# Kernel tuning notes

Measured on AMD Instinct MI355X. Metric: run time of the kernel, lower is better.

## Reference

```python
import jax, jax.numpy as jnp
import numpy as np

IMG_X, IMG_Y = 1333.0, 402.0   # image_size
MIN_SIZE = 16.0
NMS_THRESH = 0.7
PRE = 12000                    # n_train_pre_nms
POST = 2000                    # n_train_post_nms
HH, WW, A = 83, 25, 9          # 1333//16, 402//16, anchors per cell
N_ANCH = HH * WW * A           # 18675
B = 16


def setup_inputs() -> dict:
    key = jax.random.key(0)
    k1, k2, k3, k4, k5, k6 = jax.random.split(key, 6)
    # realistic anchor boxes inside the image
    xc = jax.random.uniform(k1, (N_ANCH,)) * IMG_X
    yc = jax.random.uniform(k2, (N_ANCH,)) * IMG_Y
    bw = jax.random.uniform(k3, (N_ANCH,)) * 240.0 + 16.0
    bh = jax.random.uniform(k4, (N_ANCH,)) * 120.0 + 16.0
    anchor_boxes = jnp.stack([xc - 0.5 * bw, yc - 0.5 * bh, xc + 0.5 * bw, yc + 0.5 * bh], axis=1)
    rpn_cls_score = jax.random.normal(k5, (B, N_ANCH * 2), dtype=jnp.float32)
    rpn_bbox_pred = jax.random.normal(k6, (B, N_ANCH, 4), dtype=jnp.float32) * 0.2
    return dict(anchor_boxes=anchor_boxes, rpn_cls_score=rpn_cls_score,
                rpn_bbox_pred=rpn_bbox_pred, rpn_cls_loss=jnp.zeros((1,), jnp.float32),
                rpn_bbox_loss=jnp.zeros((1,), jnp.float32))


def _decode(anchor_boxes, rpn_bbox_pred):
    ah = anchor_boxes[:, 3] - anchor_boxes[:, 1]
    aw = anchor_boxes[:, 2] - anchor_boxes[:, 0]
    acy = anchor_boxes[:, 1] + 0.5 * ah
    acx = anchor_boxes[:, 0] + 0.5 * aw
    dx = rpn_bbox_pred[..., 0]
    dy = rpn_bbox_pred[..., 1]
    dw = rpn_bbox_pred[..., 2]
    dh = rpn_bbox_pred[..., 3]
    cy = dy * ah + acy
    cx = dx * aw + acx
    h = jnp.exp(dh) * ah
    w = jnp.exp(dw) * aw
    # clip: x coords to [0, image_size[0]], y coords to [0, image_size[1]] (as in source)
    x1 = jnp.clip(cx - 0.5 * w, 0.0, IMG_X)
    y1 = jnp.clip(cy - 0.5 * h, 0.0, IMG_Y)
    x2 = jnp.clip(cx + 0.5 * w, 0.0, IMG_X)
    y2 = jnp.clip(cy + 0.5 * h, 0.0, IMG_Y)
    return jnp.stack([x1, y1, x2, y2], axis=-1)  # [N,4] broadcast over batch -> [B,N,4]


def _nms_one(roi, score):
    # roi: [N,4], score: [N]
    hs = roi[:, 3] - roi[:, 1]
    ws = roi[:, 2] - roi[:, 0]
    valid = (hs >= MIN_SIZE) & (ws >= MIN_SIZE)
    s = jnp.where(valid, score, -jnp.inf)
    idx = jnp.argsort(-s)[:PRE]          # score-descending, top pre_nms; invalid sink to end
    boxes = roi[idx]                      # score-sorted candidate boxes [PRE,4]
    vp = valid[idx]                       # which slots are real (passed size filter)
    # source quirk: order = order.argsort()[::-1] -> NMS visits boxes by DESCENDING
    # original-anchor-index; invalid slots get key -1 so they come last.
    seq_key = jnp.where(vp, idx, -1)
    perm = jnp.argsort(-seq_key)          # positions into score-sorted arrays, visit order
    x1, y1, x2, y2 = boxes[:, 0], boxes[:, 1], boxes[:, 2], boxes[:, 3]
    areas = (x2 - x1 + 1.0) * (y2 - y1 + 1.0)

    def step(alive, _):
        a_seq = alive[perm]
        any_alive = a_seq.any()
        j = perm[jnp.argmax(a_seq)]       # first surviving box in visit order
        xx1 = jnp.maximum(x1[j], x1)
        yy1 = jnp.maximum(y1[j], y1)
        xx2 = jnp.minimum(x2[j], x2)
        yy2 = jnp.minimum(y2[j], y2)
        inter = jnp.maximum(0.0, xx2 - xx1 + 1.0) * jnp.maximum(0.0, yy2 - yy1 + 1.0)
        ovr = inter / (areas[j] + areas - inter)
        alive = alive & jnp.where(any_alive, ovr <= NMS_THRESH, True)  # j kills itself (ovr=1)
        return alive, jnp.where(any_alive, j, -1)

    _, keep = jax.lax.scan(step, vp, None, length=POST)   # up to post_nms kept positions
    kmask = keep >= 0
    out = jnp.where(kmask[:, None], boxes[jnp.maximum(keep, 0)], 0.0)  # padded [POST,4]
    return out, kmask


def reference(anchor_boxes, rpn_cls_score, rpn_bbox_pred, rpn_cls_loss, rpn_bbox_loss):
    bsz = rpn_cls_score.shape[0]
    # objectness = view(B, 83, 25, 9, 2)[..., 1]
    score = rpn_cls_score.reshape(bsz, HH, WW, A, 2)[..., 1].reshape(bsz, -1)
    roi = _decode(anchor_boxes, rpn_bbox_pred)            # [B,N,4]
    rois, mask = jax.vmap(_nms_one)(roi, score)           # [B,POST,4], [B,POST]
    return rois, mask
```

## Files before the change

kernel.cpp:

```cpp
#include <hip/hip_runtime.h>
#include <math.h>

#define N_ANCHN 18675
#define NPAD    18688
#define BATCH   16
#define PRE     12000
#define CPAD    12032
#define WPB     188
#define POST    2000
#define NMS_T   0.7f
#define IMGX    1333.0f
#define IMGY    402.0f
#define MINSZ   16.0f
#define NBUCK   256
#define KINV    0x007FFFFFu
#define MLCAP   12288

typedef unsigned long long u64;

__device__ __forceinline__ unsigned key_of(float f) {
  unsigned u = __float_as_uint(f);
  return (u & 0x80000000u) ? ~u : (u | 0x80000000u);
}

__device__ __forceinline__ float iou_ref(float ax1, float ay1, float ax2, float ay2, float aar,
                                         float bx1, float by1, float bx2, float by2, float bar) {
  float xx1 = fmaxf(ax1, bx1);
  float yy1 = fmaxf(ay1, by1);
  float xx2 = fminf(ax2, bx2);
  float yy2 = fminf(ay2, by2);
  float iw = fmaxf(0.0f, __fadd_rn(__fsub_rn(xx2, xx1), 1.0f));
  float ih = fmaxf(0.0f, __fadd_rn(__fsub_rn(yy2, yy1), 1.0f));
  float inter = __fmul_rn(iw, ih);
  return __fdiv_rn(inter, __fsub_rn(__fadd_rn(aar, bar), inter));
}

__device__ __forceinline__ bool hit_test(float ix1, float iy1, float ix2, float iy2, float iar,
                                         float jx1, float jy1, float jx2, float jy2, float jar) {
  float xx1 = fmaxf(ix1, jx1);
  float yy1 = fmaxf(iy1, jy1);
  float xx2 = fminf(ix2, jx2);
  float yy2 = fminf(iy2, jy2);
  float iw = fmaxf(0.0f, __fadd_rn(__fsub_rn(xx2, xx1), 1.0f));
  float ih = fmaxf(0.0f, __fadd_rn(__fsub_rn(yy2, yy1), 1.0f));
  float inter = __fmul_rn(iw, ih);
  float S = __fadd_rn(iar, jar);
  if (inter >= __fmul_rn(0.43f, S)) return true;
  if (inter <= __fmul_rn(0.395f, S)) return false;
  return __fdiv_rn(inter, __fsub_rn(S, inter)) > NMS_T;
}

__device__ __forceinline__ void emit_hit(int lo, int hi, u64* diagb, unsigned* rcb,
                                         unsigned short* rtb, int L) {
  if ((hi >> 6) == (lo >> 6)) {
    atomicOr(&diagb[(size_t)(lo >> 6) * 64 + (lo & 63)], 1ull << (hi & 63));
  } else {
    unsigned slot = atomicAdd(&rcb[lo], 1u);
    if ((int)slot < L) rtb[(size_t)lo * L + slot] = (unsigned short)hi;
  }
}

__device__ __forceinline__ void decode_one(
    const float* __restrict__ anchors, const float* __restrict__ cls,
    const float* __restrict__ bbox, int b, int i,
    float& x1, float& y1, float& x2, float& y2, unsigned& key) {
  float4 A = *(const float4*)(anchors + (size_t)i * 4);
  float ah = __fsub_rn(A.w, A.y);
  float aw = __fsub_rn(A.z, A.x);
  float acy = __fadd_rn(A.y, __fmul_rn(0.5f, ah));
  float acx = __fadd_rn(A.x, __fmul_rn(0.5f, aw));

  float4 P = *(const float4*)(bbox + ((size_t)b * N_ANCHN + i) * 4);
  float dx = P.x, dy = P.y, dw = P.z, dh = P.w;

  float cy = __fadd_rn(__fmul_rn(dy, ah), acy);
  float cx = __fadd_rn(__fmul_rn(dx, aw), acx);
  float eh = (float)exp((double)dh);
  float ew = (float)exp((double)dw);
  float h = __fmul_rn(eh, ah);
  float w = __fmul_rn(ew, aw);

  x1 = fminf(fmaxf(__fsub_rn(cx, __fmul_rn(0.5f, w)), 0.0f), IMGX);
  y1 = fminf(fmaxf(__fsub_rn(cy, __fmul_rn(0.5f, h)), 0.0f), IMGY);
  x2 = fminf(fmaxf(__fadd_rn(cx, __fmul_rn(0.5f, w)), 0.0f), IMGX);
  y2 = fminf(fmaxf(__fadd_rn(cy, __fmul_rn(0.5f, h)), 0.0f), IMGY);

  bool valid = (__fsub_rn(y2, y1) >= MINSZ) && (__fsub_rn(x2, x1) >= MINSZ);
  float s = valid ? cls[(size_t)b * (2 * N_ANCHN) + 2 * i + 1] : -INFINITY;
  key = key_of(s);
}

__global__ __launch_bounds__(256) void decode_kernel(
    const float* __restrict__ anchors, const float* __restrict__ cls,
    const float* __restrict__ bbox,
    float* __restrict__ bx1, float* __restrict__ by1,
    float* __restrict__ bx2, float* __restrict__ by2,
    unsigned* __restrict__ keys,
    u64* __restrict__ diag, unsigned* __restrict__ rowcnt) {
  const int bx = blockIdx.x;
  const int b = blockIdx.y;
  if (bx == gridDim.x - 1) {
    u64* dz = diag + (size_t)b * WPB * 64;
    for (int i = threadIdx.x; i < WPB * 64; i += 256) dz[i] = 0ull;
    unsigned* rz = rowcnt + (size_t)b * CPAD;
    for (int i = threadIdx.x; i < CPAD; i += 256) rz[i] = 0u;
    return;
  }
  int i = bx * 256 + threadIdx.x;
  if (i >= N_ANCHN) return;
  float x1, y1, x2, y2; unsigned k;
  decode_one(anchors, cls, bbox, b, i, x1, y1, x2, y2, k);
  size_t o = (size_t)b * NPAD + i;
  bx1[o] = x1; by1[o] = y1; bx2[o] = x2; by2[o] = y2;
  keys[o] = k;
}

__global__ __launch_bounds__(1024) void prepsort_kernel(
    const unsigned* __restrict__ keys,
    const float* __restrict__ bx1, const float* __restrict__ by1,
    const float* __restrict__ bx2, const float* __restrict__ by2,
    float* __restrict__ cx1, float* __restrict__ cy1,
    float* __restrict__ cx2, float* __restrict__ cy2,
    float* __restrict__ car, int* __restrict__ ncand,
    float* __restrict__ sx1, float* __restrict__ sy1,
    float* __restrict__ sx2, float* __restrict__ sy2,
    float* __restrict__ sar, int* __restrict__ sperm,
    float* __restrict__ wminx1, float* __restrict__ wmaxx2) {
  const int b = blockIdx.x;
  const int tid = threadIdx.x;
  const int lane = tid & 63;
  const int wv = tid >> 6;
  __shared__ unsigned hist[16][256];
  __shared__ unsigned mh[256];
  __shared__ unsigned wsum[16];
  __shared__ unsigned bh[NBUCK];
  __shared__ unsigned boff[NBUCK];
  __shared__ unsigned char fb[NPAD];
  __shared__ unsigned short mlist[MLCAP];
  __shared__ unsigned sh_prefix, sh_k, sh_n, sh_mcount;
  const unsigned* kb = keys + (size_t)b * NPAD;

  if (tid == 0) { sh_prefix = 0u; sh_k = PRE; sh_mcount = 0u; }
  __syncthreads();

  {
    for (int idx = tid; idx < 16 * 256; idx += 1024) ((unsigned*)hist)[idx] = 0u;
    __syncthreads();
    for (int i = tid; i < N_ANCHN; i += 1024)
      atomicAdd(&hist[wv][kb[i] >> 24], 1u);
    __syncthreads();
    if (tid < 256) {
      unsigned s = 0;
#pragma unroll
      for (int q = 0; q < 16; ++q) s += hist[q][tid];
      mh[tid] = s;
    }
    __syncthreads();
    if (tid == 0) {
      unsigned kk = sh_k, cum = 0;
      for (int d = 255; d >= 0; --d) {
        unsigned c = mh[d];
        if (cum + c >= kk) { sh_k = kk - cum; sh_prefix = (unsigned)d << 24; break; }
        cum += c;
      }
    }
    __syncthreads();
  }

  {
    unsigned b0 = sh_prefix >> 24;
    for (int i = tid; i < N_ANCHN; i += 1024) {
      if ((kb[i] >> 24) == b0) {
        unsigned p = atomicAdd(&sh_mcount, 1u);
        if (p < MLCAP) mlist[p] = (unsigned short)i;
      }
    }
  }
  __syncthreads();
  const bool useList = (sh_mcount <= (unsigned)MLCAP);
  const unsigned mcount = min(sh_mcount, (unsigned)MLCAP);

  for (int level = 1; level < 4; ++level) {
    const int shift = 24 - 8 * level;
    for (int idx = tid; idx < 16 * 256; idx += 1024) ((unsigned*)hist)[idx] = 0u;
    __syncthreads();
    unsigned pre = sh_prefix;
    if (useList) {
      for (int idx = tid; idx < (int)mcount; idx += 1024) {
        unsigned k = kb[mlist[idx]];
        if ((k >> (shift + 8)) == (pre >> (shift + 8)))
          atomicAdd(&hist[wv][(k >> shift) & 255u], 1u);
      }
    } else {
      for (int i = tid; i < N_ANCHN; i += 1024) {
        unsigned k = kb[i];
        if ((k >> (shift + 8)) == (pre >> (shift + 8)))
          atomicAdd(&hist[wv][(k >> shift) & 255u], 1u);
      }
    }
    __syncthreads();
    if (tid < 256) {
      unsigned s = 0;
#pragma unroll
      for (int q = 0; q < 16; ++q) s += hist[q][tid];
      mh[tid] = s;
    }
    __syncthreads();
    if (tid == 0) {
      unsigned kk = sh_k, cum = 0;
      for (int d = 255; d >= 0; --d) {
        unsigned c = mh[d];
        if (cum + c >= kk) { sh_k = kk - cum; sh_prefix = pre | ((unsigned)d << shift); break; }
        cum += c;
      }
    }
    __syncthreads();
  }
  const unsigned T = sh_prefix;
  const unsigned slots = sh_k;

  const int SEG = (N_ANCHN + 1023) / 1024;

  {
    int i0 = tid * SEG, i1 = min(N_ANCHN, i0 + SEG);
    unsigned cnt = 0;
    for (int i = i0; i < i1; ++i) cnt += (kb[i] == T) ? 1u : 0u;
    unsigned v = cnt;
#pragma unroll
    for (int d = 1; d < 64; d <<= 1) {
      unsigned y = __shfl_up(v, d, 64);
      if (lane >= d) v += y;
    }
    if (lane == 63) wsum[wv] = v;
    __syncthreads();
    if (tid == 0) {
      unsigned acc = 0;
#pragma unroll
      for (int q = 0; q < 16; ++q) { unsigned t = wsum[q]; wsum[q] = acc; acc += t; }
    }
    __syncthreads();
    unsigned r = wsum[wv] + v - cnt;
    for (int i = i0; i < i1; ++i) {
      unsigned k = kb[i];
      bool tie = (k == T);
      bool cand = (k > T) || (tie && T > KINV && r < slots);
      if (tie) r++;
      fb[i] = cand ? (unsigned char)1 : (unsigned char)0;
    }
  }
  __syncthreads();

  const float* X1 = bx1 + (size_t)b * NPAD;
  const float* Y1 = by1 + (size_t)b * NPAD;
  const float* X2 = bx2 + (size_t)b * NPAD;
  const float* Y2 = by2 + (size_t)b * NPAD;
  {
    int j0 = tid * SEG, j1 = min(N_ANCHN, j0 + SEG);
    unsigned cnt = 0;
    for (int j = j0; j < j1; ++j) cnt += fb[N_ANCHN - 1 - j];
    unsigned v = cnt;
#pragma unroll
    for (int d = 1; d < 64; d <<= 1) {
      unsigned y = __shfl_up(v, d, 64);
      if (lane >= d) v += y;
    }
    if (lane == 63) wsum[wv] = v;
    __syncthreads();
    if (tid == 0) {
      unsigned acc = 0;
#pragma unroll
      for (int q = 0; q < 16; ++q) { unsigned t = wsum[q]; wsum[q] = acc; acc += t; }
      sh_n = acc;
    }
    __syncthreads();
    unsigned p = wsum[wv] + v - cnt;
    if (tid == 0) ncand[b] = (int)sh_n;
    float* CX1 = cx1 + (size_t)b * CPAD;
    float* CY1 = cy1 + (size_t)b * CPAD;
    float* CX2 = cx2 + (size_t)b * CPAD;
    float* CY2 = cy2 + (size_t)b * CPAD;
    float* CAR = car + (size_t)b * CPAD;
    for (int j = j0; j < j1; ++j) {
      int i = N_ANCHN - 1 - j;
      if (fb[i]) {
        float x1v = X1[i], y1v = Y1[i], x2v = X2[i], y2v = Y2[i];
        CX1[p] = x1v; CY1[p] = y1v; CX2[p] = x2v; CY2[p] = y2v;
        CAR[p] = __fmul_rn(__fadd_rn(__fsub_rn(x2v, x1v), 1.0f),
                           __fadd_rn(__fsub_rn(y2v, y1v), 1.0f));
        p++;
      }
    }
  }
  __syncthreads();
  const int n = (int)sh_n;

  const float scale = (float)NBUCK / 1334.0f;
  const float* CX1 = cx1 + (size_t)b * CPAD;
  const float* CY1 = cy1 + (size_t)b * CPAD;
  const float* CX2 = cx2 + (size_t)b * CPAD;
  const float* CY2 = cy2 + (size_t)b * CPAD;
  const float* CAR = car + (size_t)b * CPAD;
  float* SX1 = sx1 + (size_t)b * CPAD;
  float* SY1 = sy1 + (size_t)b * CPAD;
  float* SX2 = sx2 + (size_t)b * CPAD;
  float* SY2 = sy2 + (size_t)b * CPAD;
  float* SAR = sar + (size_t)b * CPAD;
  int* SP = sperm + (size_t)b * CPAD;

  if (tid < NBUCK) bh[tid] = 0u;
  __syncthreads();
  for (int i = tid; i < n; i += 1024) {
    int q = (int)(CX1[i] * scale);
    q = q < 0 ? 0 : (q > NBUCK - 1 ? NBUCK - 1 : q);
    atomicAdd(&bh[q], 1u);
  }
  __syncthreads();
  if (tid < 64) {
    unsigned carry = 0;
    for (int c = 0; c < 4; ++c) {
      unsigned own = bh[c * 64 + tid];
      unsigned v = own;
      for (int d = 1; d < 64; d <<= 1) {
        unsigned y = __shfl_up(v, d, 64);
        if (tid >= d) v += y;
      }
      boff[c * 64 + tid] = carry + v - own;
      carry += __shfl(v, 63, 64);
    }
  }
  __syncthreads();
  for (int i = tid; i < n; i += 1024) {
    float x1v = CX1[i];
    int q = (int)(x1v * scale);
    q = q < 0 ? 0 : (q > NBUCK - 1 ? NBUCK - 1 : q);
    unsigned p = atomicAdd(&boff[q], 1u);
    SX1[p] = x1v; SY1[p] = CY1[i]; SX2[p] = CX2[i]; SY2[p] = CY2[i];
    SAR[p] = CAR[i]; SP[p] = i;
  }
  for (int i = n + tid; i < CPAD; i += 1024) {
    SX1[i] = 1e30f; SY1[i] = 1e30f; SX2[i] = -1e30f; SY2[i] = -1e30f;
    SAR[i] = 1.0f; SP[i] = 0;
  }
  __syncthreads();
  for (int w = wv; w < WPB; w += 16) {
    float mn = SX1[64 * w + lane];
    float mx = SX2[64 * w + lane];
#pragma unroll
    for (int d = 32; d > 0; d >>= 1) {
      mn = fminf(mn, __shfl_xor(mn, d, 64));
      mx = fmaxf(mx, __shfl_xor(mx, d, 64));
    }
    if (lane == 0) {
      wminx1[(size_t)b * WPB + w] = mn;
      wmaxx2[(size_t)b * WPB + w] = mx;
    }
  }
}

__global__ __launch_bounds__(256) void build_kernel(
    const float* __restrict__ sx1, const float* __restrict__ sy1,
    const float* __restrict__ sx2, const float* __restrict__ sy2,
    const float* __restrict__ sar, const int* __restrict__ sperm,
    const int* __restrict__ ncand,
    const float* __restrict__ wminx1, const float* __restrict__ wmaxx2,
    u64* __restrict__ diagT, unsigned* __restrict__ rowcnt,
    unsigned short* __restrict__ rows_t, int L) {
  const int R = blockIdx.x, G0 = blockIdx.y, b = blockIdx.z;
  const int n = ncand[b];
  if (64 * R >= n) return;
  if (16 * G0 + 15 < R) return;
  const float* WMN = wminx1 + (size_t)b * WPB;
  const float rlim = __fadd_rn(wmaxx2[(size_t)b * WPB + R], 2.0f);
  {
    const int wlo = max(16 * G0, R);
    if (WMN[wlo] > __fadd_rn(rlim, 5.25f)) return;
  }

  const float* SX1 = sx1 + (size_t)b * CPAD;
  const float* SY1 = sy1 + (size_t)b * CPAD;
  const float* SX2 = sx2 + (size_t)b * CPAD;
  const float* SY2 = sy2 + (size_t)b * CPAD;
  const float* SAR = sar + (size_t)b * CPAD;
  const int* SP = sperm + (size_t)b * CPAD;

  const int t = threadIdx.x, lane = t & 63, q = t >> 6;

  __shared__ float4 rbv[64];
  __shared__ float2 ras[64];
  if (t < 64) {
    int i = 64 * R + t;
    rbv[t] = make_float4(SX1[i], SY1[i], SX2[i], SY2[i]);
  } else if (t < 128) {
    int i = 64 * R + (t - 64);
    ras[t - 64] = make_float2(SAR[i], __int_as_float(SP[i]));
  }
  const float rx2own = SX2[64 * R + lane];
  __syncthreads();

  const int w0 = 16 * G0 + 4 * q;
  const float wmn0 = WMN[min(w0 + 0, WPB - 1)];
  const float wmn1 = WMN[min(w0 + 1, WPB - 1)];
  const float wmn2 = WMN[min(w0 + 2, WPB - 1)];
  const float wmn3 = WMN[min(w0 + 3, WPB - 1)];
  const bool v0 = (w0 + 0 < WPB) && (w0 + 0 >= R) && (wmn0 <= rlim);
  const bool v1 = (w0 + 1 < WPB) && (w0 + 1 >= R) && (wmn1 <= rlim);
  const bool v2 = (w0 + 2 < WPB) && (w0 + 2 >= R) && (wmn2 <= rlim);
  const bool v3 = (w0 + 3 < WPB) && (w0 + 3 >= R) && (wmn3 <= rlim);
  if (!(v0 | v1 | v2 | v3)) return;

  float c0x1 = 1e30f, c0y1 = 0.f, c0x2 = 0.f, c0y2 = 0.f, c0ar = 1.f; int c0sp = 0;
  float c1x1 = 1e30f, c1y1 = 0.f, c1x2 = 0.f, c1y2 = 0.f, c1ar = 1.f; int c1sp = 0;
  float c2x1 = 1e30f, c2y1 = 0.f, c2x2 = 0.f, c2y2 = 0.f, c2ar = 1.f; int c2sp = 0;
  float c3x1 = 1e30f, c3y1 = 0.f, c3x2 = 0.f, c3y2 = 0.f, c3ar = 1.f; int c3sp = 0;
  if (v0) { int j = 64 * (w0 + 0) + lane;
    c0x1 = SX1[j]; c0y1 = SY1[j]; c0x2 = SX2[j]; c0y2 = SY2[j]; c0ar = SAR[j]; c0sp = SP[j]; }
  if (v1) { int j = 64 * (w0 + 1) + lane;
    c1x1 = SX1[j]; c1y1 = SY1[j]; c1x2 = SX2[j]; c1y2 = SY2[j]; c1ar = SAR[j]; c1sp = SP[j]; }
  if (v2) { int j = 64 * (w0 + 2) + lane;
    c2x1 = SX1[j]; c2y1 = SY1[j]; c2x2 = SX2[j]; c2y2 = SY2[j]; c2ar = SAR[j]; c2sp = SP[j]; }
  if (v3) { int j = 64 * (w0 + 3) + lane;
    c3x1 = SX1[j]; c3y1 = SY1[j]; c3x2 = SX2[j]; c3y2 = SY2[j]; c3ar = SAR[j]; c3sp = SP[j]; }

  const float wmnlo = v0 ? wmn0 : (v1 ? wmn1 : (v2 ? wmn2 : wmn3));
  u64 a = __ballot(rx2own >= __fsub_rn(wmnlo, 2.0f));
  if (!a) return;

  const float wmn0m2 = __fsub_rn(wmn0, 2.0f);
  const float wmn1m2 = __fsub_rn(wmn1, 2.0f);
  const float wmn2m2 = __fsub_rn(wmn2, 2.0f);
  const float wmn3m2 = __fsub_rn(wmn3, 2.0f);

  u64* diagb = diagT + (size_t)b * WPB * 64;
  unsigned* rcb = rowcnt + (size_t)b * CPAD;
  unsigned short* rtb = rows_t + (size_t)b * L * CPAD;

  const bool diagIn = (w0 <= R) & (R <= w0 + 3);
  if (!diagIn) {
    int k = (int)__builtin_ctzll(a);
    float4 RB = rbv[k];
    float2 AS = ras[k];
    while (true) {
      a &= a - 1;
      const int kn = a ? (int)__builtin_ctzll(a) : 0;
      const float4 RBn = rbv[kn];
      const float2 ASn = ras[kn];
      const float rx2k = RB.z;
      const float rark = AS.x;
      const int rsp = __float_as_int(AS.y);
      if (v0 && rx2k >= wmn0m2 &&
          hit_test(RB.x, RB.y, RB.z, RB.w, rark, c0x1, c0y1, c0x2, c0y2, c0ar))
        emit_hit(min(rsp, c0sp), max(rsp, c0sp), diagb, rcb, rtb, L);
      if (v1 && rx2k >= wmn1m2 &&
          hit_test(RB.x, RB.y, RB.z, RB.w, rark, c1x1, c1y1, c1x2, c1y2, c1ar))
        emit_hit(min(rsp, c1sp), max(rsp, c1sp), diagb, rcb, rtb, L);
      if (v2 && rx2k >= wmn2m2 &&
          hit_test(RB.x, RB.y, RB.z, RB.w, rark, c2x1, c2y1, c2x2, c2y2, c2ar))
        emit_hit(min(rsp, c2sp), max(rsp, c2sp), diagb, rcb, rtb, L);
      if (v3 && rx2k >= wmn3m2 &&
          hit_test(RB.x, RB.y, RB.z, RB.w, rark, c3x1, c3y1, c3x2, c3y2, c3ar))
        emit_hit(min(rsp, c3sp), max(rsp, c3sp), diagb, rcb, rtb, L);
      if (!a) break;
      RB = RBn; AS = ASn;
    }
  } else {
    const bool g0 = (w0 + 0 > R), e0 = (w0 + 0 == R);
    const bool g1 = (w0 + 1 > R), e1 = (w0 + 1 == R);
    const bool g2 = (w0 + 2 > R), e2 = (w0 + 2 == R);
    const bool g3 = (w0 + 3 > R), e3 = (w0 + 3 == R);
    int k = (int)__builtin_ctzll(a);
    float4 RB = rbv[k];
    float2 AS = ras[k];
    while (true) {
      a &= a - 1;
      const int kn = a ? (int)__builtin_ctzll(a) : 0;
      const float4 RBn = rbv[kn];
      const float2 ASn = ras[kn];
      const float rx2k = RB.z;
      const float rark = AS.x;
      const int rsp = __float_as_int(AS.y);
      if (v0 && rx2k >= wmn0m2) {
        bool dd = g0 | (e0 & (lane > k));
        if (dd && hit_test(RB.x, RB.y, RB.z, RB.w, rark, c0x1, c0y1, c0x2, c0y2, c0ar))
          emit_hit(min(rsp, c0sp), max(rsp, c0sp), diagb, rcb, rtb, L);
      }
      if (v1 && rx2k >= wmn1m2) {
        bool dd = g1 | (e1 & (lane > k));
        if (dd && hit_test(RB.x, RB.y, RB.z, RB.w, rark, c1x1, c1y1, c1x2, c1y2, c1ar))
          emit_hit(min(rsp, c1sp), max(rsp, c1sp), diagb, rcb, rtb, L);
      }
      if (v2 && rx2k >= wmn2m2) {
        bool dd = g2 | (e2 & (lane > k));
        if (dd && hit_test(RB.x, RB.y, RB.z, RB.w, rark, c2x1, c2y1, c2x2, c2y2, c2ar))
          emit_hit(min(rsp, c2sp), max(rsp, c2sp), diagb, rcb, rtb, L);
      }
      if (v3 && rx2k >= wmn3m2) {
        bool dd = g3 | (e3 & (lane > k));
        if (dd && hit_test(RB.x, RB.y, RB.z, RB.w, rark, c3x1, c3y1, c3x2, c3y2, c3ar))
          emit_hit(min(rsp, c3sp), max(rsp, c3sp), diagb, rcb, rtb, L);
      }
      if (!a) break;
      k = kn; RB = RBn; AS = ASn;
    }
  }
}

#define DECLW(s) u64 kw##s; unsigned cw##s; uint4 p0##s, p1##s;
#define LOADW(s, wexp) { int w_ = (wexp); int c_ = 64 * w_ + lane; \
  kw##s = diagb[(size_t)w_ * 64 + lane]; cw##s = rcb[c_]; \
  const uint4* rp_ = (const uint4*)(rtb + (size_t)c_ * L); p0##s = rp_[0]; p1##s = rp_[1]; }
#define PROCW(s, wexp) { int w_ = (wexp); \
  if (w_ < nw && sc < POST) { \
    const int base_ = 64 * w_; const int myc_ = base_ + lane; \
    const u64 suppw_ = supp[w_]; \
    const bool alv_ = (myc_ < n) && !((suppw_ >> lane) & 1ull); \
    u64 act_ = __ballot(alv_); \
    u64 selw_ = 0ull; \
    const int scb_ = sc; \
    const unsigned klo_ = (unsigned)kw##s, khi_ = (unsigned)(kw##s >> 32); \
    while (act_ && sc < POST) { \
      const int j_ = (int)__builtin_ctzll(act_); \
      const u64 kj_ = ((u64)(unsigned)__builtin_amdgcn_readlane((int)khi_, j_) << 32) | \
                      (u64)(unsigned)__builtin_amdgcn_readlane((int)klo_, j_); \
      selw_ |= 1ull << j_; sc++; \
      act_ &= ~(kj_ | (1ull << j_)); } \
    const bool selme_ = ((selw_ >> lane) & 1ull) != 0ull; \
    if (selme_) { \
      const int rank_ = scb_ + (int)__popcll(selw_ & ((1ull << lane) - 1ull)); \
      sel[rank_] = myc_; \
      const int ce_ = min((int)cw##s, L); \
      uint4 p2_ = {0,0,0,0}, p3_ = {0,0,0,0}; \
      if (ce_ > 16) { \
        const uint4* rp_ = (const uint4*)(rtb + (size_t)myc_ * L); \
        p2_ = rp_[2]; p3_ = rp_[3]; \
      } \
      unsigned ev_[8] = {p0##s.x, p0##s.y, p0##s.z, p0##s.w, p1##s.x, p1##s.y, p1##s.z, p1##s.w}; \
      _Pragma("unroll") \
      for (int u_ = 0; u_ < 8; ++u_) { \
        if (2 * u_ < ce_)     { int t_ = (int)(ev_[u_] & 0xffffu); atomicOr(&supp[t_ >> 6], 1ull << (t_ & 63)); } \
        if (2 * u_ + 1 < ce_) { int t_ = (int)(ev_[u_] >> 16);     atomicOr(&supp[t_ >> 6], 1ull << (t_ & 63)); } } \
      if (ce_ > 16) { \
        unsigned e2_[8] = {p2_.x, p2_.y, p2_.z, p2_.w, p3_.x, p3_.y, p3_.z, p3_.w}; \
        _Pragma("unroll") \
        for (int u_ = 0; u_ < 8; ++u_) { \
          if (16 + 2 * u_ < ce_)     { int t_ = (int)(e2_[u_] & 0xffffu); atomicOr(&supp[t_ >> 6], 1ull << (t_ & 63)); } \
          if (16 + 2 * u_ + 1 < ce_) { int t_ = (int)(e2_[u_] >> 16);     atomicOr(&supp[t_ >> 6], 1ull << (t_ & 63)); } } } \
      for (int e_ = 32; e_ < ce_; ++e_) { \
        int t_ = (int)rtb[(size_t)myc_ * L + e_]; atomicOr(&supp[t_ >> 6], 1ull << (t_ & 63)); } } \
    u64 om_ = __ballot(selme_ && ((int)cw##s > L)); \
    while (om_) { \
      int j_ = (int)__builtin_ctzll(om_); om_ &= om_ - 1; \
      const int mc_ = base_ + j_; \
      float ax1_ = CX1[mc_], ay1_ = CY1[mc_], ax2_ = CX2[mc_], ay2_ = CY2[mc_], aar_ = CAR[mc_]; \
      const float xhi_ = __fadd_rn(ax2_, 2.0f); \
      const float xlo_ = __fsub_rn(ax1_, 2.0f); \
      for (int w2_ = 0; w2_ < nw; ++w2_) { \
        if (WMN[w2_] > xhi_) break; \
        if (WMX[w2_] < xlo_) continue; \
        int sj_ = 64 * w2_ + lane; \
        float ovr_ = iou_ref(ax1_, ay1_, ax2_, ay2_, aar_, \
                             SX1[sj_], SY1[sj_], SX2[sj_], SY2[sj_], SAR[sj_]); \
        if (ovr_ > NMS_T) { \
          int cj_ = SP[sj_]; \
          if (cj_ >= base_ + 64) atomicOr(&supp[cj_ >> 6], 1ull << (cj_ & 63)); } } } } }

#define LOADG(s, gexp) { int g_ = (gexp); \
  LOADW(s##0, min(4 * g_ + 0, WPB - 1)) \
  LOADW(s##1, min(4 * g_ + 1, WPB - 1)) \
  LOADW(s##2, min(4 * g_ + 2, WPB - 1)) \
  LOADW(s##3, min(4 * g_ + 3, WPB - 1)) }
#define PROCG(s, gexp) { int gg_ = (gexp); \
  PROCW(s##0, 4 * gg_ + 0) \
  PROCW(s##1, 4 * gg_ + 1) \
  PROCW(s##2, 4 * gg_ + 2) \
  PROCW(s##3, 4 * gg_ + 3) }

__global__ __launch_bounds__(64) void scan_kernel(
    const float* __restrict__ cx1, const float* __restrict__ cy1,
    const float* __restrict__ cx2, const float* __restrict__ cy2,
    const float* __restrict__ car, const int* __restrict__ ncand,
    const float* __restrict__ sx1, const float* __restrict__ sy1,
    const float* __restrict__ sx2, const float* __restrict__ sy2,
    const float* __restrict__ sar, const int* __restrict__ sperm,
    const float* __restrict__ wminx1, const float* __restrict__ wmaxx2,
    const u64* __restrict__ diagT, const unsigned* __restrict__ rowcnt,
    const unsigned short* __restrict__ rows_t, int L,
    float* __restrict__ out) {
  const int b = blockIdx.x;
  const int lane = threadIdx.x;
  __shared__ u64 supp[WPB];
  __shared__ int sel[POST];
  for (int idx = lane; idx < WPB; idx += 64) supp[idx] = 0ull;

  const int n = ncand[b];
  const u64* diagb = diagT + (size_t)b * WPB * 64;
  const unsigned* rcb = rowcnt + (size_t)b * CPAD;
  const unsigned short* rtb = rows_t + (size_t)b * L * CPAD;
  const float* CX1 = cx1 + (size_t)b * CPAD;
  const float* CY1 = cy1 + (size_t)b * CPAD;
  const float* CX2 = cx2 + (size_t)b * CPAD;
  const float* CY2 = cy2 + (size_t)b * CPAD;
  const float* CAR = car + (size_t)b * CPAD;
  const float* SX1 = sx1 + (size_t)b * CPAD;
  const float* SY1 = sy1 + (size_t)b * CPAD;
  const float* SX2 = sx2 + (size_t)b * CPAD;
  const float* SY2 = sy2 + (size_t)b * CPAD;
  const float* SAR = sar + (size_t)b * CPAD;
  const int* SP = sperm + (size_t)b * CPAD;
  const float* WMN = wminx1 + (size_t)b * WPB;
  const float* WMX = wmaxx2 + (size_t)b * WPB;

  const int nw = (n + 63) >> 6;
  int sc = 0;

  DECLW(a0) DECLW(a1) DECLW(a2) DECLW(a3)
  DECLW(b0) DECLW(b1) DECLW(b2) DECLW(b3)
  DECLW(c0) DECLW(c1) DECLW(c2) DECLW(c3)

  if (nw > 0) {
    LOADG(a, 0)
    LOADG(b, 1)
    LOADG(c, 2)
    const int ng = (nw + 3) >> 2;
    for (int g = 0; g < ng && sc < POST; g += 3) {
      PROCG(a, g)
      LOADG(a, g + 3)
      PROCG(b, g + 1)
      LOADG(b, g + 4)
      PROCG(c, g + 2)
      LOADG(c, g + 5)
    }
  }

  float* roib = out + (size_t)b * POST * 4;
  float* maskb = out + (size_t)BATCH * POST * 4 + (size_t)b * POST;
  for (int t = lane; t < POST; t += 64) {
    if (t < sc) {
      int j = sel[t];
      float4 v = make_float4(CX1[j], CY1[j], CX2[j], CY2[j]);
      *(float4*)(roib + (size_t)t * 4) = v;
      maskb[t] = 1.0f;
    } else {
      *(float4*)(roib + (size_t)t * 4) = make_float4(0.f, 0.f, 0.f, 0.f);
      maskb[t] = 0.0f;
    }
  }
}

__global__ __launch_bounds__(256) void decode_fb_kernel(
    const float* __restrict__ anchors, const float* __restrict__ cls,
    const float* __restrict__ bbox,
    float* __restrict__ bx1, float* __restrict__ by1,
    float* __restrict__ bx2, float* __restrict__ by2,
    unsigned* __restrict__ keys) {
  int i = blockIdx.x * 256 + threadIdx.x;
  if (i >= N_ANCHN) return;
  int b = blockIdx.y;
  float x1, y1, x2, y2; unsigned k;
  decode_one(anchors, cls, bbox, b, i, x1, y1, x2, y2, k);
  size_t o = (size_t)b * NPAD + i;
  bx1[o] = x1; by1[o] = y1; bx2[o] = x2; by2[o] = y2;
  keys[o] = k;
}

__global__ __launch_bounds__(1024) void prep_kernel(
    const unsigned* __restrict__ keys,
    const float* __restrict__ bx1, const float* __restrict__ by1,
    const float* __restrict__ bx2, const float* __restrict__ by2,
    unsigned char* __restrict__ flags,
    float* __restrict__ cx1, float* __restrict__ cy1,
    float* __restrict__ cx2, float* __restrict__ cy2,
    float* __restrict__ car, int* __restrict__ ncand) {
  const int b = blockIdx.x;
  const int tid = threadIdx.x;
  __shared__ unsigned hist[256];
  __shared__ unsigned ssc[1024];
  __shared__ unsigned sh_prefix, sh_k;
  const unsigned* kb = keys + (size_t)b * NPAD;

  if (tid == 0) { sh_prefix = 0u; sh_k = PRE; }
  __syncthreads();

  for (int level = 0; level < 4; ++level) {
    const int shift = 24 - 8 * level;
    if (tid < 256) hist[tid] = 0u;
    __syncthreads();
    unsigned pre = sh_prefix;
    for (int i = tid; i < N_ANCHN; i += 1024) {
      unsigned k = kb[i];
      bool match = (level == 0) || ((k >> (shift + 8)) == (pre >> (shift + 8)));
      if (match) atomicAdd(&hist[(k >> shift) & 255u], 1u);
    }
    __syncthreads();
    if (tid == 0) {
      unsigned kk = sh_k, cum = 0;
      for (int d = 255; d >= 0; --d) {
        unsigned c = hist[d];
        if (cum + c >= kk) { sh_k = kk - cum; sh_prefix = pre | ((unsigned)d << shift); break; }
        cum += c;
      }
    }
    __syncthreads();
  }
  const unsigned T = sh_prefix;

  unsigned local = 0;
  for (int i = tid; i < N_ANCHN; i += 1024) local += (kb[i] > T) ? 1u : 0u;
  ssc[tid] = local;
  __syncthreads();
  for (int off = 512; off > 0; off >>= 1) {
    if (tid < off) ssc[tid] += ssc[tid + off];
    __syncthreads();
  }
  const unsigned slots = PRE - ssc[0];
  __syncthreads();

  const int SEG = (N_ANCHN + 1023) / 1024;
  const float* X1 = bx1 + (size_t)b * NPAD;
  const float* Y1 = by1 + (size_t)b * NPAD;
  const float* X2 = bx2 + (size_t)b * NPAD;
  const float* Y2 = by2 + (size_t)b * NPAD;
  unsigned char* fb = flags + (size_t)b * NPAD;

  {
    int i0 = tid * SEG, i1 = min(N_ANCHN, i0 + SEG);
    unsigned cnt = 0;
    for (int i = i0; i < i1; ++i) cnt += (kb[i] == T) ? 1u : 0u;
    ssc[tid] = cnt;
    __syncthreads();
    for (int off = 1; off < 1024; off <<= 1) {
      unsigned v = (tid >= off) ? ssc[tid - off] : 0u;
      __syncthreads();
      ssc[tid] += v;
      __syncthreads();
    }
    unsigned r = ssc[tid] - cnt;
    for (int i = i0; i < i1; ++i) {
      unsigned k = kb[i];
      bool valid = (__fsub_rn(Y2[i], Y1[i]) >= MINSZ) && (__fsub_rn(X2[i], X1[i]) >= MINSZ);
      bool tie = (k == T);
      bool cand = valid && ((k > T) || (tie && r < slots));
      if (tie) r++;
      fb[i] = cand ? (unsigned char)1 : (unsigned char)0;
    }
  }
  __syncthreads();

  {
    int j0 = tid * SEG, j1 = min(N_ANCHN, j0 + SEG);
    unsigned cnt = 0;
    for (int j = j0; j < j1; ++j) cnt += fb[N_ANCHN - 1 - j];
    ssc[tid] = cnt;
    __syncthreads();
    for (int off = 1; off < 1024; off <<= 1) {
      unsigned v = (tid >= off) ? ssc[tid - off] : 0u;
      __syncthreads();
      ssc[tid] += v;
      __syncthreads();
    }
    unsigned p = ssc[tid] - cnt;
    if (tid == 0) ncand[b] = (int)ssc[1023];
    float* CX1 = cx1 + (size_t)b * CPAD;
    float* CY1 = cy1 + (size_t)b * CPAD;
    float* CX2 = cx2 + (size_t)b * CPAD;
    float* CY2 = cy2 + (size_t)b * CPAD;
    float* CAR = car + (size_t)b * CPAD;
    for (int j = j0; j < j1; ++j) {
      int i = N_ANCHN - 1 - j;
      if (fb[i]) {
        float x1v = X1[i], y1v = Y1[i], x2v = X2[i], y2v = Y2[i];
        CX1[p] = x1v; CY1[p] = y1v; CX2[p] = x2v; CY2[p] = y2v;
        CAR[p] = __fmul_rn(__fadd_rn(__fsub_rn(x2v, x1v), 1.0f),
                           __fadd_rn(__fsub_rn(y2v, y1v), 1.0f));
        p++;
      }
    }
  }
}

__global__ __launch_bounds__(1024) void nms_kernel(
    const float* __restrict__ cx1, const float* __restrict__ cy1,
    const float* __restrict__ cx2, const float* __restrict__ cy2,
    const float* __restrict__ car, const int* __restrict__ ncand,
    float* __restrict__ out) {
  const int b = blockIdx.x;
  const int tid = threadIdx.x;
  __shared__ float sx1[POST], sy1[POST], sx2[POST], sy2[POST], sar[POST];
  __shared__ int Lbuf[1024];
  __shared__ int wcount[16];
  __shared__ int sh_sc;

  const float* CX1 = cx1 + (size_t)b * CPAD;
  const float* CY1 = cy1 + (size_t)b * CPAD;
  const float* CX2 = cx2 + (size_t)b * CPAD;
  const float* CY2 = cy2 + (size_t)b * CPAD;
  const float* CAR = car + (size_t)b * CPAD;
  float* roib = out + (size_t)b * POST * 4;
  float* maskb = out + (size_t)BATCH * POST * 4 + (size_t)b * POST;

  const int n = ncand[b];
  if (tid == 0) sh_sc = 0;
  __syncthreads();
  const int lane = tid & 63;
  const int w = tid >> 6;

  for (int base = 0; base < n; base += 1024) {
    const int c = base + tid;
    bool pass = (c < n);
    float px1 = 0, py1 = 0, px2 = 0, py2 = 0, par = 0;
    if (pass) { px1 = CX1[c]; py1 = CY1[c]; px2 = CX2[c]; py2 = CY2[c]; par = CAR[c]; }
    const int sc0 = sh_sc;

    if (pass) {
      for (int k = 0; k < sc0; ++k) {
        float ovr = iou_ref(sx1[k], sy1[k], sx2[k], sy2[k], sar[k], px1, py1, px2, py2, par);
        if (ovr > NMS_T) { pass = false; break; }
      }
    }

    unsigned long long bal = __ballot(pass);
    if (lane == 0) wcount[w] = (int)__popcll(bal);
    __syncthreads();
    int off = 0;
    for (int q = 0; q < 16; ++q) off += (q < w) ? wcount[q] : 0;
    if (pass) Lbuf[off + (int)__popcll(bal & ((1ULL << lane) - 1ULL))] = c;
    __syncthreads();

    if (tid < 64) {
      int total = 0;
      for (int q = 0; q < 16; ++q) total += wcount[q];
      int sc = sc0;
      for (int g = 0; g < total && sc < POST; g += 64) {
        int idx = (g + lane < total) ? Lbuf[g + lane] : -1;
        float qx1 = 0, qy1 = 0, qx2 = 0, qy2 = 0, qar = 0;
        bool al = (idx >= 0);
        if (al) { qx1 = CX1[idx]; qy1 = CY1[idx]; qx2 = CX2[idx]; qy2 = CY2[idx]; qar = CAR[idx]; }
        for (int k = sc0; k < sc && al; ++k) {
          float ovr = iou_ref(sx1[k], sy1[k], sx2[k], sy2[k], sar[k], qx1, qy1, qx2, qy2, qar);
          if (ovr > NMS_T) al = false;
        }
        unsigned long long alive = __ballot(al);
        while (alive && sc < POST) {
          int j = (int)__builtin_ctzll(alive);
          float jx1 = __shfl(qx1, j), jy1 = __shfl(qy1, j);
          float jx2 = __shfl(qx2, j), jy2 = __shfl(qy2, j), jar = __shfl(qar, j);
          float ovr = iou_ref(jx1, jy1, jx2, jy2, jar, qx1, qy1, qx2, qy2, qar);
          unsigned long long killm = __ballot(ovr > NMS_T);
          alive &= ~killm;
          alive &= ~(1ULL << j);
          if (lane == 0) {
            sx1[sc] = jx1; sy1[sc] = jy1; sx2[sc] = jx2; sy2[sc] = jy2; sar[sc] = jar;
            roib[(size_t)sc * 4 + 0] = jx1;
            roib[(size_t)sc * 4 + 1] = jy1;
            roib[(size_t)sc * 4 + 2] = jx2;
            roib[(size_t)sc * 4 + 3] = jy2;
          }
          sc++;
        }
      }
      if (lane == 0) sh_sc = sc;
    }
    __syncthreads();
    if (sh_sc >= POST) break;
  }
  __syncthreads();

  const int sc = sh_sc;
  for (int t = tid; t < POST; t += 1024) {
    if (t >= sc) {
      roib[(size_t)t * 4 + 0] = 0.f; roib[(size_t)t * 4 + 1] = 0.f;
      roib[(size_t)t * 4 + 2] = 0.f; roib[(size_t)t * 4 + 3] = 0.f;
    }
    maskb[t] = (t < sc) ? 1.0f : 0.0f;
  }
}

extern "C" void kernel_launch(void* const* d_in, const int* in_sizes, int n_in,
                              void* d_out, int out_size, void* d_ws, size_t ws_size,
                              hipStream_t stream) {
  const float* anchors = (const float*)d_in[0];
  const float* cls = (const float*)d_in[1];
  const float* bbox = (const float*)d_in[2];
  float* out = (float*)d_out;
  char* ws = (char*)d_ws;

  size_t o = 0;
  float* cx1 = (float*)(ws + o); o += (size_t)BATCH * CPAD * 4;
  float* cy1 = (float*)(ws + o); o += (size_t)BATCH * CPAD * 4;
  float* cx2 = (float*)(ws + o); o += (size_t)BATCH * CPAD * 4;
  float* cy2 = (float*)(ws + o); o += (size_t)BATCH * CPAD * 4;
  float* car = (float*)(ws + o); o += (size_t)BATCH * CPAD * 4;
  int* ncand = (int*)(ws + o); o += 256;
  u64* diag = (u64*)(ws + o); o += (size_t)BATCH * WPB * 64 * 8;
  unsigned* rowcnt = (unsigned*)(ws + o); o += (size_t)BATCH * CPAD * 4;
  float* wminx1 = (float*)(ws + o); o += (size_t)BATCH * WPB * 4;
  float* wmaxx2 = (float*)(ws + o); o += (size_t)BATCH * WPB * 4;
  float* sx1 = (float*)(ws + o); o += (size_t)BATCH * CPAD * 4;
  float* sy1 = (float*)(ws + o); o += (size_t)BATCH * CPAD * 4;
  float* sx2 = (float*)(ws + o); o += (size_t)BATCH * CPAD * 4;
  float* sy2 = (float*)(ws + o); o += (size_t)BATCH * CPAD * 4;
  float* sar = (float*)(ws + o); o += (size_t)BATCH * CPAD * 4;
  int* sperm = (int*)(ws + o); o += (size_t)BATCH * CPAD * 4;
  size_t overlay = o;
  unsigned* keys = (unsigned*)(ws + overlay);
  float* bx1 = (float*)(ws + overlay + (size_t)BATCH * NPAD * 4 * 1);
  float* by1 = (float*)(ws + overlay + (size_t)BATCH * NPAD * 4 * 2);
  float* bx2 = (float*)(ws + overlay + (size_t)BATCH * NPAD * 4 * 3);
  float* by2 = (float*)(ws + overlay + (size_t)BATCH * NPAD * 4 * 4);
  size_t decode_bytes = (size_t)BATCH * NPAD * 4 * 5;
  unsigned short* rows_t = (unsigned short*)(ws + overlay);

  int L = 0;
  for (int Ltry = 64; Ltry >= 16; Ltry >>= 1) {
    size_t rows_bytes = (size_t)BATCH * Ltry * CPAD * 2;
    size_t need = overlay + (decode_bytes > rows_bytes ? decode_bytes : rows_bytes);
    if (ws_size >= need) { L = Ltry; break; }
  }

  if (L > 0) {
    dim3 dgrid((N_ANCHN + 255) / 256 + 1, BATCH);
    decode_kernel<<<dgrid, 256, 0, stream>>>(anchors, cls, bbox, bx1, by1, bx2, by2,
                                             keys, diag, rowcnt);
    prepsort_kernel<<<BATCH, 1024, 0, stream>>>(keys, bx1, by1, bx2, by2,
                                                cx1, cy1, cx2, cy2, car, ncand,
                                                sx1, sy1, sx2, sy2, sar, sperm,
                                                wminx1, wmaxx2);
    build_kernel<<<dim3(WPB, (WPB + 15) / 16, BATCH), 256, 0, stream>>>(
        sx1, sy1, sx2, sy2, sar, sperm, ncand, wminx1, wmaxx2,
        diag, rowcnt, rows_t, L);
    scan_kernel<<<BATCH, 64, 0, stream>>>(cx1, cy1, cx2, cy2, car, ncand,
                                          sx1, sy1, sx2, sy2, sar, sperm,
                                          wminx1, wmaxx2,
                                          diag, rowcnt, rows_t, L, out);
  } else {
    size_t f = 0;
    unsigned* fkeys = (unsigned*)(ws + f); f += (size_t)BATCH * NPAD * 4;
    float* fbx1 = (float*)(ws + f); f += (size_t)BATCH * NPAD * 4;
    float* fby1 = (float*)(ws + f); f += (size_t)BATCH * NPAD * 4;
    float* fbx2 = (float*)(ws + f); f += (size_t)BATCH * NPAD * 4;
    float* fby2 = (float*)(ws + f); f += (size_t)BATCH * NPAD * 4;
    float* fcx1 = (float*)(ws + f); f += (size_t)BATCH * CPAD * 4;
    float* fcy1 = (float*)(ws + f); f += (size_t)BATCH * CPAD * 4;
    float* fcx2 = (float*)(ws + f); f += (size_t)BATCH * CPAD * 4;
    float* fcy2 = (float*)(ws + f); f += (size_t)BATCH * CPAD * 4;
    float* fcar = (float*)(ws + f); f += (size_t)BATCH * CPAD * 4;
    unsigned char* fflags = (unsigned char*)(ws + f); f += (size_t)BATCH * NPAD;
    int* fncand = (int*)(ws + f); f += 256;

    dim3 dgrid((N_ANCHN + 255) / 256, BATCH);
    decode_fb_kernel<<<dgrid, 256, 0, stream>>>(anchors, cls, bbox, fbx1, fby1, fbx2, fby2, fkeys);
    prep_kernel<<<BATCH, 1024, 0, stream>>>(fkeys, fbx1, fby1, fbx2, fby2, fflags,
                                            fcx1, fcy1, fcx2, fcy2, fcar, fncand);
    nms_kernel<<<BATCH, 1024, 0, stream>>>(fcx1, fcy1, fcx2, fcy2, fcar, fncand, out);
  }
}
```

Baseline: 533.1 us.

## Fuse top-byte histogram into decode, store boxes as float4, drop scan ballot

The decode kernel now writes each box as one float4 and accumulates the per-batch top-byte key histogram with global atomics. This lets the single-block-per-batch prepsort kernel skip its own histogram pass and gather candidates with one vector load. In the NMS scan, the active-lane mask is derived from the uniform suppression word via readfirstlane instead of a ballot. The cost is global atomic contention on a few hot bins and an extra memset launch.

Measured after the change: 635.6 us. 19.2% more time.

```diff
diff --git a/kernel.cpp b/kernel.cpp
--- a/kernel.cpp
+++ b/kernel.cpp
@@ -93,9 +93,8 @@
 __global__ __launch_bounds__(256) void decode_kernel(
     const float* __restrict__ anchors, const float* __restrict__ cls,
     const float* __restrict__ bbox,
-    float* __restrict__ bx1, float* __restrict__ by1,
-    float* __restrict__ bx2, float* __restrict__ by2,
-    unsigned* __restrict__ keys,
+    float4* __restrict__ bbox4, unsigned* __restrict__ keys,
+    unsigned* __restrict__ ghist,
     u64* __restrict__ diag, unsigned* __restrict__ rowcnt) {
   const int bx = blockIdx.x;
   const int b = blockIdx.y;
@@ -111,14 +110,14 @@
   float x1, y1, x2, y2; unsigned k;
   decode_one(anchors, cls, bbox, b, i, x1, y1, x2, y2, k);
   size_t o = (size_t)b * NPAD + i;
-  bx1[o] = x1; by1[o] = y1; bx2[o] = x2; by2[o] = y2;
+  bbox4[o] = make_float4(x1, y1, x2, y2);
   keys[o] = k;
+  atomicAdd(&ghist[b * 256 + (k >> 24)], 1u);
 }
 
 __global__ __launch_bounds__(1024) void prepsort_kernel(
-    const unsigned* __restrict__ keys,
-    const float* __restrict__ bx1, const float* __restrict__ by1,
-    const float* __restrict__ bx2, const float* __restrict__ by2,
+    const unsigned* __restrict__ keys, const float4* __restrict__ bbox4,
+    const unsigned* __restrict__ ghist,
     float* __restrict__ cx1, float* __restrict__ cy1,
     float* __restrict__ cx2, float* __restrict__ cy2,
     float* __restrict__ car, int* __restrict__ ncand,
@@ -144,17 +143,7 @@
   __syncthreads();
 
   {
-    for (int idx = tid; idx < 16 * 256; idx += 1024) ((unsigned*)hist)[idx] = 0u;
-    __syncthreads();
-    for (int i = tid; i < N_ANCHN; i += 1024)
-      atomicAdd(&hist[wv][kb[i] >> 24], 1u);
-    __syncthreads();
-    if (tid < 256) {
-      unsigned s = 0;
-#pragma unroll
-      for (int q = 0; q < 16; ++q) s += hist[q][tid];
-      mh[tid] = s;
-    }
+    if (tid < 256) mh[tid] = ghist[b * 256 + tid];
     __syncthreads();
     if (tid == 0) {
       unsigned kk = sh_k, cum = 0;
@@ -250,10 +239,7 @@
   }
   __syncthreads();
 
-  const float* X1 = bx1 + (size_t)b * NPAD;
-  const float* Y1 = by1 + (size_t)b * NPAD;
-  const float* X2 = bx2 + (size_t)b * NPAD;
-  const float* Y2 = by2 + (size_t)b * NPAD;
+  const float4* BB4 = bbox4 + (size_t)b * NPAD;
   {
     int j0 = tid * SEG, j1 = min(N_ANCHN, j0 + SEG);
     unsigned cnt = 0;
@@ -283,10 +269,10 @@
     for (int j = j0; j < j1; ++j) {
       int i = N_ANCHN - 1 - j;
       if (fb[i]) {
-        float x1v = X1[i], y1v = Y1[i], x2v = X2[i], y2v = Y2[i];
-        CX1[p] = x1v; CY1[p] = y1v; CX2[p] = x2v; CY2[p] = y2v;
-        CAR[p] = __fmul_rn(__fadd_rn(__fsub_rn(x2v, x1v), 1.0f),
-                           __fadd_rn(__fsub_rn(y2v, y1v), 1.0f));
+        float4 v4 = BB4[i];
+        CX1[p] = v4.x; CY1[p] = v4.y; CX2[p] = v4.z; CY2[p] = v4.w;
+        CAR[p] = __fmul_rn(__fadd_rn(__fsub_rn(v4.z, v4.x), 1.0f),
+                           __fadd_rn(__fsub_rn(v4.w, v4.y), 1.0f));
         p++;
       }
     }
@@ -512,8 +498,11 @@
   if (w_ < nw && sc < POST) { \
     const int base_ = 64 * w_; const int myc_ = base_ + lane; \
     const u64 suppw_ = supp[w_]; \
-    const bool alv_ = (myc_ < n) && !((suppw_ >> lane) & 1ull); \
-    u64 act_ = __ballot(alv_); \
+    const unsigned slo_ = (unsigned)__builtin_amdgcn_readfirstlane((int)(unsigned)suppw_); \
+    const unsigned shi_ = (unsigned)__builtin_amdgcn_readfirstlane((int)(unsigned)(suppw_ >> 32)); \
+    u64 act_ = ~(((u64)shi_ << 32) | (u64)slo_); \
+    const int rem_ = n - base_; \
+    if (rem_ < 64) act_ &= ((1ull << rem_) - 1ull); \
     u64 selw_ = 0ull; \
     const int scb_ = sc; \
     const unsigned klo_ = (unsigned)kw##s, khi_ = (unsigned)(kw##s >> 32); \
@@ -894,6 +883,7 @@
   unsigned* rowcnt = (unsigned*)(ws + o); o += (size_t)BATCH * CPAD * 4;
   float* wminx1 = (float*)(ws + o); o += (size_t)BATCH * WPB * 4;
   float* wmaxx2 = (float*)(ws + o); o += (size_t)BATCH * WPB * 4;
+  unsigned* ghist = (unsigned*)(ws + o); o += (size_t)BATCH * 256 * 4;
   float* sx1 = (float*)(ws + o); o += (size_t)BATCH * CPAD * 4;
   float* sy1 = (float*)(ws + o); o += (size_t)BATCH * CPAD * 4;
   float* sx2 = (float*)(ws + o); o += (size_t)BATCH * CPAD * 4;
@@ -902,10 +892,7 @@
   int* sperm = (int*)(ws + o); o += (size_t)BATCH * CPAD * 4;
   size_t overlay = o;
   unsigned* keys = (unsigned*)(ws + overlay);
-  float* bx1 = (float*)(ws + overlay + (size_t)BATCH * NPAD * 4 * 1);
-  float* by1 = (float*)(ws + overlay + (size_t)BATCH * NPAD * 4 * 2);
-  float* bx2 = (float*)(ws + overlay + (size_t)BATCH * NPAD * 4 * 3);
-  float* by2 = (float*)(ws + overlay + (size_t)BATCH * NPAD * 4 * 4);
+  float4* bbox4 = (float4*)(ws + overlay + (size_t)BATCH * NPAD * 4);
   size_t decode_bytes = (size_t)BATCH * NPAD * 4 * 5;
   unsigned short* rows_t = (unsigned short*)(ws + overlay);
 
@@ -917,10 +904,11 @@
   }
 
   if (L > 0) {
+    hipMemsetAsync(ghist, 0, (size_t)BATCH * 256 * 4, stream);
     dim3 dgrid((N_ANCHN + 255) / 256 + 1, BATCH);
-    decode_kernel<<<dgrid, 256, 0, stream>>>(anchors, cls, bbox, bx1, by1, bx2, by2,
-                                             keys, diag, rowcnt);
-    prepsort_kernel<<<BATCH, 1024, 0, stream>>>(keys, bx1, by1, bx2, by2,
+    decode_kernel<<<dgrid, 256, 0, stream>>>(anchors, cls, bbox, bbox4, keys,
+                                             ghist, diag, rowcnt);
+    prepsort_kernel<<<BATCH, 1024, 0, stream>>>(keys, bbox4, ghist,
                                                 cx1, cy1, cx2, cy2, car, ncand,
                                                 sx1, sy1, sx2, sy2, sar, sperm,
                                                 wminx1, wmaxx2);
```
